# Performance work log

Measured on AMD Instinct MI355X. Metric: run time of the kernel, lower is better.

The kernel has to match this reference:

```python
import jax, jax.numpy as jnp
import numpy as np


def _u(k, shape, s):
    return jax.random.uniform(k, shape, jnp.float32, -s, s)


def setup_inputs() -> dict:
    B, T, F, H = 256, 256, 128, 256
    key = jax.random.key(0)
    ks = jax.random.split(key, 40)
    sH = 1.0 / np.sqrt(H).astype(np.float32)
    sF = 1.0 / np.sqrt(F).astype(np.float32)
    s2F = 1.0 / np.sqrt(2 * F).astype(np.float32)
    s3F = 1.0 / np.sqrt(3 * F).astype(np.float32)
    d = {
        'x': jax.random.normal(ks[0], (B, T, F), jnp.float32),
        'masking': (jax.random.uniform(ks[1], (B, T, F)) < 0.8).astype(jnp.float32),
        'time_lag': jax.random.uniform(ks[2], (B, T, F), jnp.float32),
        # forward LSTMCell (torch layout: W_ih [4H,2F], W_hh [4H,H], gates i,f,g,o)
        'fw_Wih': _u(ks[3], (4 * H, 2 * F), sH), 'fw_Whh': _u(ks[4], (4 * H, H), sH),
        'fw_bih': _u(ks[5], (4 * H,), sH), 'fw_bhh': _u(ks[6], (4 * H,), sH),
        'bw_Wih': _u(ks[7], (4 * H, 2 * F), sH), 'bw_Whh': _u(ks[8], (4 * H, H), sH),
        'bw_bih': _u(ks[9], (4 * H,), sH), 'bw_bhh': _u(ks[10], (4 * H,), sH),
        'fwlin_W': _u(ks[11], (F, H), sH), 'fwlin_b': _u(ks[12], (F,), sH),
        'bwlin_W': _u(ks[13], (F, H), sH), 'bwlin_b': _u(ks[14], (F,), sH),
        'fwz_W': _u(ks[15], (F, F), sF), 'fwz_b': _u(ks[16], (F,), sF),
        'bwz_W': _u(ks[17], (F, F), sF), 'bwz_b': _u(ks[18], (F,), sF),
        # beta linear 2F -> 3F
        'fwbeta_W': _u(ks[19], (3 * F, 2 * F), s2F), 'fwbeta_b': _u(ks[20], (3 * F,), s2F),
        'bwbeta_W': _u(ks[21], (3 * F, 2 * F), s2F), 'bwbeta_b': _u(ks[22], (3 * F,), s2F),
        # time-lag decay F -> H (both directions)
        'lag_W': _u(ks[23], (H, F), sF), 'lag_b': _u(ks[24], (H,), sF),
        'lagb_W': _u(ks[25], (H, F), sF), 'lagb_b': _u(ks[26], (H,), sF),
        # r_beta H -> F (both directions)
        'rbeta_W': _u(ks[27], (F, H), sH), 'rbeta_b': _u(ks[28], (F,), sH),
        'rbetab_W': _u(ks[29], (F, H), sH), 'rbetab_b': _u(ks[30], (F,), sH),
        # shared linear_layer_test 3F -> F
        'test_W': _u(ks[31], (F, 3 * F), s3F), 'test_b': _u(ks[32], (F,), s3F),
    }
    return d


def _lstm_cell(inp, h, c, Wih, Whh, bih, bhh):
    g = inp @ Wih.T + bih + h @ Whh.T + bhh
    i, f, gg, o = jnp.split(g, 4, axis=-1)
    c2 = jax.nn.sigmoid(f) * c + jax.nn.sigmoid(i) * jnp.tanh(gg)
    h2 = jax.nn.sigmoid(o) * jnp.tanh(c2)
    return h2, c2


def _run_dir(x, m, rr, rb, lin_W, lin_b, z_W, z_b, beta_W, beta_b, test_W, test_b, Wih, Whh, bih, bhh):
    # x, m: [T,B,F]; rr: [T,B,H]; rb: [T,B,F]
    F = x.shape[-1]
    offdiag = 1.0 - jnp.eye(F, dtype=x.dtype)

    def step(carry, inp):
        h, c = carry
        xj, mj, rj, rbj = inp
        out = h @ lin_W.T + lin_b                                 # [B,F]
        x_c = mj * xj + (1.0 - mj) * out
        z = x_c @ (z_W * offdiag).T + z_b
        beta = jax.nn.sigmoid(jnp.concatenate([mj, rbj], -1) @ beta_W.T + beta_b)
        beta = beta @ test_W.T + test_b                           # [B,F]
        c_val = beta * z + (1.0 - beta) * out
        c_c = mj * xj + (1.0 - mj) * c_val
        h2, c2 = _lstm_cell(jnp.concatenate([c_c, mj], -1), h * rj, c, Wih, Whh, bih, bhh)
        return (h2, c2), (out, z, c_val)

    bs, H = x.shape[1], Whh.shape[-1]
    h0 = jnp.zeros((bs, H), x.dtype)
    _, (outs, zs, cs) = jax.lax.scan(step, (h0, h0), (x, m, rr, rb))
    return outs, zs, cs


def reference(x, masking, time_lag, fw_Wih, fw_Whh, fw_bih, fw_bhh, bw_Wih, bw_Whh, bw_bih, bw_bhh, fwlin_W, fwlin_b, bwlin_W, bwlin_b, fwz_W, fwz_b, bwz_W, bwz_b, fwbeta_W, fwbeta_b, bwbeta_W, bwbeta_b, lag_W, lag_b, lagb_W, lagb_b, rbeta_W, rbeta_b, rbetab_W, rbetab_b, test_W, test_b):
    xt = jnp.transpose(x, (1, 0, 2))         # [T,B,F]
    mt = jnp.transpose(masking, (1, 0, 2))
    lt = jnp.transpose(time_lag, (1, 0, 2))
    # forward direction decay
    rr_f = jnp.exp(-jax.nn.relu(lt @ lag_W.T + lag_b))            # [T,B,H]
    rb_f = rr_f @ rbeta_W.T + rbeta_b                             # [T,B,F]
    of, zf, cf = _run_dir(xt, mt, rr_f, rb_f, fwlin_W, fwlin_b, fwz_W, fwz_b,
                          fwbeta_W, fwbeta_b, test_W, test_b, fw_Wih, fw_Whh, fw_bih, fw_bhh)
    # backward direction: iterate time reversed, then un-reverse outputs
    rr_b = jnp.exp(-jax.nn.relu(lt @ lagb_W.T + lagb_b))
    rb_b = rr_b @ rbetab_W.T + rbetab_b
    rev = lambda a: a[::-1]
    ob, zb, cb = _run_dir(rev(xt), rev(mt), rev(rr_b), rev(rb_b), bwlin_W, bwlin_b,
                          bwz_W, bwz_b, bwbeta_W, bwbeta_b, test_W, test_b,
                          bw_Wih, bw_Whh, bw_bih, bw_bhh)
    ob, zb, cb = rev(ob), rev(zb), rev(cb)
    perm = lambda a: jnp.transpose(a, (1, 0, 2))                  # back to [B,T,F]
    return (perm(of), perm(zf), perm(cf), perm(ob), perm(zb), perm(cb))
```

## Files before the change

### kernel.cpp

```cpp
#include <hip/hip_runtime.h>
#include <stdint.h>

#define TT 256
#define FF 128
#define HH 256
#define BB 256
#define BTc (BB * TT)
#define BTFc ((size_t)BB * TT * FF)

typedef __attribute__((ext_vector_type(8))) short short8;
typedef __attribute__((ext_vector_type(4))) float floatx4;
typedef __attribute__((ext_vector_type(4))) int intx4;

__device__ __forceinline__ floatx4 mfma16(short8 a, short8 b, floatx4 c) {
    return __builtin_amdgcn_mfma_f32_16x16x32_bf16(a, b, c, 0, 0, 0);
}
__device__ __forceinline__ intx4 mfmai8(long a, long b, intx4 c) {
    return __builtin_amdgcn_mfma_i32_16x16x32_i8(a, b, c, 0, 0, 0);
}

__device__ __forceinline__ float bf2f(short s) {
    return __uint_as_float(((unsigned)(unsigned short)s) << 16);
}
__device__ __forceinline__ short f2bf(float f) {
    unsigned u = __float_as_uint(f);
    u += 0x7FFFu + ((u >> 16) & 1u);
    return (short)(u >> 16);
}
__device__ __forceinline__ short8 ld_cvt8(const float* __restrict__ p) {
    short8 r;
#pragma unroll
    for (int j = 0; j < 8; ++j) r[j] = f2bf(p[j]);
    return r;
}
__device__ __forceinline__ float sigf(float x) { return 1.f / (1.f + __expf(-x)); }
__device__ __forceinline__ float tanhf_(float x) { return 1.f - 2.f / (1.f + __expf(2.f * x)); }

#define BARSYNC() do { asm volatile("s_waitcnt lgkmcnt(0)" ::: "memory"); \
                       __builtin_amdgcn_s_barrier(); } while (0)

struct PrepArgs {
    const float *s0, *s1, *s2, *s3, *s4, *s5, *s6;
    short *d0, *d1, *d2, *d3, *d4, *d5, *d6;
};
struct ScaleDesc { const float* src; int stride; int coloff; int K; int nrows; int sbase; };
struct ScaleArgs { ScaleDesc d[6]; float* s; };
struct PackBDesc { const float* src; short* dst; int stride; int coloff; int kts; int diag; int groups; };
struct AArgs { PrepArgs p; ScaleArgs s; PackBDesc b[6]; };

__global__ __launch_bounds__(256) void k_a(AArgs A) {
    if (blockIdx.x < 1472) {
        int i = blockIdx.x * 256 + threadIdx.x;
        const PrepArgs& P = A.p;
        if (i < 32768) { P.d0[i] = f2bf(P.s0[i]); return; }  i -= 32768;
        if (i < 32768) { P.d1[i] = f2bf(P.s1[i]); return; }  i -= 32768;
        if (i < 32768) { P.d2[i] = f2bf(P.s2[i]); return; }  i -= 32768;
        if (i < 32768) { P.d3[i] = f2bf(P.s3[i]); return; }  i -= 32768;
        if (i < 98304) { P.d4[i] = f2bf(P.s4[i]); return; }  i -= 98304;
        if (i < 98304) { P.d5[i] = f2bf(P.s5[i]); return; }  i -= 98304;
        if (i < 49152) { P.d6[i] = f2bf(P.s6[i]); return; }
        return;
    }
    if (blockIdx.x < 2560) {
        int gw = ((blockIdx.x - 1472) * 256 + threadIdx.x) >> 6;
        int lane = threadIdx.x & 63;
#pragma unroll 1
        for (int i = 0; i < 6; ++i) {
            if (gw < A.s.d[i].nrows) {
                const float* p = A.s.d[i].src + (size_t)gw * A.s.d[i].stride + A.s.d[i].coloff;
                float amax = 0.f;
                for (int j = lane; j < A.s.d[i].K; j += 64) amax = fmaxf(amax, fabsf(p[j]));
#pragma unroll
                for (int off = 32; off; off >>= 1) amax = fmaxf(amax, __shfl_xor(amax, off, 64));
                if (lane == 0) A.s.s[A.s.d[i].sbase + gw] = fmaxf(amax, 1e-20f);
                return;
            }
            gw -= A.s.d[i].nrows;
        }
        return;
    }
    int g = (blockIdx.x - 2560) * 256 + threadIdx.x;
#pragma unroll 1
    for (int i = 0; i < 6; ++i) {
        const PackBDesc& D = A.b[i];
        if (g < D.groups) {
            int frag = g >> 6, lane = g & 63;
            int nt = frag >> 2, kt = frag & 3;
            int ln = lane & 15, q4 = lane >> 4;
            int row = nt * 16 + ln;
            const float* p = D.src + (size_t)row * D.stride + D.coloff + kt * 32 + q4 * 8;
            short* dp = D.dst + (size_t)g * 8;
#pragma unroll
            for (int j = 0; j < 8; ++j) {
                int col = kt * 32 + q4 * 8 + j;
                float v = p[j];
                if (D.diag && col == row) v = 0.f;
                dp[j] = f2bf(v);
            }
            return;
        }
        g -= D.groups;
    }
}

struct PackQDesc { const float* src; char* dst; int stride; int coloff; int kts; int sbase; int groups; };
struct BArgs {
    const float* lt;
    const short* lagW0; const float* lagb0; const short* rbW0; const float* rbb0;
    short* rr0; short* rb0;
    const short* lagW1; const float* lagb1; const short* rbW1; const float* rbb1;
    short* rr1; short* rb1;
    const float* m;
    const short* wmB0; const short* wmB1;
    short* gb0; short* gb1;
    PackQDesc q[4]; const float* s;
};

__global__ __launch_bounds__(256) void k_b(BArgs A) {
    __shared__ short rrS[128][264];
    const int tid = threadIdx.x, lane = tid & 63, w = tid >> 6;
    const int ln = lane & 15, q4 = lane >> 4;

    if (blockIdx.x < 1024) {
        int b = blockIdx.x;
        const int dir = b >> 9; b &= 511;
        const int tc  = b & 7;
        const int q4d = (b >> 3) & 3;
        const int bg  = b >> 5;
        const short* lagW = dir ? A.lagW1 : A.lagW0;
        const float* lagb = dir ? A.lagb1 : A.lagb0;
        const short* rbW  = dir ? A.rbW1  : A.rbW0;
        const float* rbb  = dir ? A.rbb1  : A.rbb0;
        short* rr = dir ? A.rr1 : A.rr0;
        short* rb = dir ? A.rb1 : A.rb0;

#pragma unroll
        for (int mt = 0; mt < 2; ++mt) {
            const int rbase = w * 32 + mt * 16;
            floatx4 acc[16];
#pragma unroll
            for (int nt = 0; nt < 16; ++nt) { floatx4 z = {0.f, 0.f, 0.f, 0.f}; acc[nt] = z; }
            const int r = rbase + ln;
            const size_t aoff = ((size_t)(bg * 16 + q4d * 4 + (r >> 5)) * TT + tc * 32 + (r & 31)) * FF;
#pragma unroll
            for (int kt = 0; kt < 4; ++kt) {
                short8 a = ld_cvt8(A.lt + aoff + kt * 32 + q4 * 8);
#pragma unroll
                for (int nt = 0; nt < 16; ++nt) {
                    short8 bfr = *(const short8*)(lagW + (nt * 16 + ln) * 128 + kt * 32 + q4 * 8);
                    acc[nt] = mfma16(a, bfr, acc[nt]);
                }
            }
#pragma unroll
            for (int nt = 0; nt < 16; ++nt) {
                int n = nt * 16 + ln;
                float bias = lagb[n];
#pragma unroll
                for (int r2 = 0; r2 < 4; ++r2) {
                    int row = rbase + q4 * 4 + r2;
                    rrS[row][n] = f2bf(__expf(-fmaxf(acc[nt][r2] + bias, 0.f)));
                }
            }
        }
        __syncthreads();
        for (int c = tid; c < 32 * 256; c += 256) {
            int tl = c >> 8, n = c & 255;
            unsigned long long pk =
                ((unsigned long long)(unsigned short)rrS[tl][n]) |
                ((unsigned long long)(unsigned short)rrS[32 + tl][n] << 16) |
                ((unsigned long long)(unsigned short)rrS[64 + tl][n] << 32) |
                ((unsigned long long)(unsigned short)rrS[96 + tl][n] << 48);
            size_t doff = ((((size_t)(bg * TT + tc * 32 + tl) * 16 + (n >> 4)) * 64)
                           + q4d * 16 + (n & 15)) * 4;
            *(unsigned long long*)(rr + doff) = pk;
        }
#pragma unroll
        for (int mt = 0; mt < 2; ++mt) {
            const int rbase = w * 32 + mt * 16;
            floatx4 acc[8];
#pragma unroll
            for (int nt = 0; nt < 8; ++nt) { floatx4 z = {0.f, 0.f, 0.f, 0.f}; acc[nt] = z; }
#pragma unroll
            for (int kt = 0; kt < 8; ++kt) {
                short8 a = *(const short8*)&rrS[rbase + ln][kt * 32 + q4 * 8];
#pragma unroll
                for (int nt = 0; nt < 8; ++nt) {
                    short8 bfr = *(const short8*)(rbW + (nt * 16 + ln) * 256 + kt * 32 + q4 * 8);
                    acc[nt] = mfma16(a, bfr, acc[nt]);
                }
            }
#pragma unroll
            for (int nt = 0; nt < 8; ++nt) {
                int n = nt * 16 + ln;
                float bias = rbb[n];
#pragma unroll
                for (int r2 = 0; r2 < 4; ++r2) {
                    int row = rbase + q4 * 4 + r2;
                    size_t roff = ((size_t)(bg * 16 + q4d * 4 + (row >> 5)) * TT
                                   + tc * 32 + (row & 31)) * 128;
                    rb[roff + n] = f2bf(acc[nt][r2] + bias);
                }
            }
        }
        return;
    }

    if (blockIdx.x < 3072) {
        int task = (blockIdx.x - 1024) * 4 + w;
        const int dir = task >> 12; task &= 4095;
        const int bg = task >> 8, t = task & 255;
        const short* wB = dir ? A.wmB1 : A.wmB0;
        short* gb = dir ? A.gb1 : A.gb0;

        short8 a[4];
#pragma unroll
        for (int kt = 0; kt < 4; ++kt)
            a[kt] = ld_cvt8(A.m + ((size_t)(bg * 16 + ln) * TT + t) * FF + kt * 32 + q4 * 8);

        short* dst = gb + (size_t)task * 16384 + lane * 4;
#pragma unroll 2
        for (int nt = 0; nt < 64; ++nt) {
            floatx4 acc = {0.f, 0.f, 0.f, 0.f};
#pragma unroll
            for (int kt = 0; kt < 4; ++kt) {
                short8 bfr = *(const short8*)(wB + (nt * 4 + kt) * 512 + lane * 8);
                acc = mfma16(a[kt], bfr, acc);
            }
            unsigned long long pk =
                ((unsigned long long)(unsigned short)f2bf(acc[0])) |
                ((unsigned long long)(unsigned short)f2bf(acc[1]) << 16) |
                ((unsigned long long)(unsigned short)f2bf(acc[2]) << 32) |
                ((unsigned long long)(unsigned short)f2bf(acc[3]) << 48);
            *(unsigned long long*)(dst + nt * 256) = pk;
        }
        return;
    }

    int g = (blockIdx.x - 3072) * 256 + tid;
#pragma unroll 1
    for (int i = 0; i < 4; ++i) {
        const PackQDesc& D = A.q[i];
        if (g < D.groups) {
            int frag = g >> 6, plane = g & 63;
            int nt = frag / D.kts, kt = frag - nt * D.kts;
            int pln = plane & 15, pq4 = plane >> 4;
            int row = nt * 16 + pln;
            const float* p = D.src + (size_t)row * D.stride + D.coloff + kt * 32 + pq4 * 8;
            float inv = 127.f / A.s[D.sbase + row];
            char* dp = D.dst + (size_t)g * 8;
#pragma unroll
            for (int j = 0; j < 8; ++j) {
                int q = __float2int_rn(p[j] * inv);
                q = q > 127 ? 127 : (q < -127 ? -127 : q);
                dp[j] = (char)q;
            }
            return;
        }
        g -= D.groups;
    }
}

__global__ __launch_bounds__(256) void k_beta2(
    const float* __restrict__ m,
    const short* __restrict__ rb0, const short* __restrict__ rb1,
    const short* __restrict__ bW0, const short* __restrict__ bW1,
    const float* __restrict__ bb0, const float* __restrict__ bb1,
    const short* __restrict__ tW, const float* __restrict__ tb,
    short* __restrict__ bout0, short* __restrict__ bout1) {
    __shared__ short uS[64][392];
    const int tid = threadIdx.x, lane = tid & 63, w = tid >> 6;
    const int ln = lane & 15, q4 = lane >> 4;
    const int dir = blockIdx.x >> 10;
    const size_t r0 = (size_t)(blockIdx.x & 1023) * 64;
    const short* rb = dir ? rb1 : rb0;
    const short* bW = dir ? bW1 : bW0;
    const float* bb = dir ? bb1 : bb0;
    short* bout = dir ? bout1 : bout0;
    const int rbase = w * 16;

    {
        floatx4 acc[24];
#pragma unroll
        for (int nt = 0; nt < 24; ++nt) { floatx4 z = {0.f, 0.f, 0.f, 0.f}; acc[nt] = z; }
#pragma unroll
        for (int kt = 0; kt < 8; ++kt) {
            short8 a;
            if (kt < 4) a = ld_cvt8(m + (r0 + rbase + ln) * 128 + kt * 32 + q4 * 8);
            else        a = *(const short8*)(rb + (r0 + rbase + ln) * 128 + (kt - 4) * 32 + q4 * 8);
#pragma unroll
            for (int nt = 0; nt < 24; ++nt) {
                short8 b = *(const short8*)(bW + (nt * 16 + ln) * 256 + kt * 32 + q4 * 8);
                acc[nt] = mfma16(a, b, acc[nt]);
            }
        }
#pragma unroll
        for (int nt = 0; nt < 24; ++nt) {
            int n = nt * 16 + ln;
            float bias = bb[n];
#pragma unroll
            for (int r = 0; r < 4; ++r)
                uS[rbase + q4 * 4 + r][n] = f2bf(sigf(acc[nt][r] + bias));
        }
    }
    __syncthreads();
    {
        floatx4 acc[8];
#pragma unroll
        for (int nt = 0; nt < 8; ++nt) { floatx4 z = {0.f, 0.f, 0.f, 0.f}; acc[nt] = z; }
#pragma unroll
        for (int kt = 0; kt < 12; ++kt) {
            short8 a = *(const short8*)&uS[rbase + ln][kt * 32 + q4 * 8];
#pragma unroll
            for (int nt = 0; nt < 8; ++nt) {
                short8 b = *(const short8*)(tW + (nt * 16 + ln) * 384 + kt * 32 + q4 * 8);
                acc[nt] = mfma16(a, b, acc[nt]);
            }
        }
#pragma unroll
        for (int nt = 0; nt < 8; ++nt) {
            int n = nt * 16 + ln;
            float bias = tb[n];
#pragma unroll
            for (int r = 0; r < 4; ++r)
                bout[(r0 + rbase + q4 * 4 + r) * 128 + n] = f2bf(acc[nt][r] + bias);
        }
    }
}

struct ScanArgs {
    const float* x; const float* m;
    const short* rr0; const short* rr1;
    const short* beta0; const short* beta1;
    const short* gb0; const short* gb1;
    const char* whh0; const char* whh1;
    const char* lin0; const char* lin1;
    const short* wihc0; const short* wihc1;
    const short* zw0; const short* zw1;
    const float* s_all;
    const float* bih0; const float* bhh0; const float* bih1; const float* bhh1;
    const float* linb0; const float* linb1; const float* zb0; const float* zb1;
    float* out;
};

__global__ __launch_bounds__(1024, 4) void k_scan(ScanArgs A) {
    const int tid = threadIdx.x;
    const int lane = tid & 63;
    const int w = tid >> 6;
    const int ln = lane & 15;
    const int q4 = lane >> 4;
    const int dir = blockIdx.x >> 4;
    const int bgi = blockIdx.x & 15;
    const int bg0 = bgi * 16;

    const short* rrF   = dir ? A.rr1   : A.rr0;
    const short* beta  = dir ? A.beta1 : A.beta0;
    const short* gbF   = dir ? A.gb1   : A.gb0;
    const char*  whhQ  = dir ? A.whh1  : A.whh0;
    const char*  linQ  = dir ? A.lin1  : A.lin0;
    const short* wihcB = dir ? A.wihc1 : A.wihc0;
    const short* zwB   = dir ? A.zw1   : A.zw0;
    const float* bih   = dir ? A.bih1  : A.bih0;
    const float* bhh   = dir ? A.bhh1  : A.bhh0;
    const float* linb  = dir ? A.linb1 : A.linb0;
    const float* zb    = dir ? A.zb1   : A.zb0;
    const int so_whh  = dir ? 1024 : 0;
    const int so_lin  = 4096 + (dir ? 128 : 0);

    __shared__ char  hS8[16][264];
    __shared__ char  hrS8[16][264];
    __shared__ char  msS8[16][136];
    __shared__ short xS[16][136];
    __shared__ short bS[16][136];
    __shared__ short outS[16][136];
    __shared__ short ccS[16][136];
    __shared__ short zwS[16384];
    __shared__ char  linS8[32768];

    long WhhP[4][8];
#pragma unroll
    for (int q = 0; q < 4; ++q)
#pragma unroll
        for (int kt = 0; kt < 8; ++kt)
            WhhP[q][kt] = *(const long*)(whhQ + (((w + 16 * q) * 8 + kt) * 512 + lane * 8));

    float fhh[4], gb[4];
#pragma unroll
    for (int q = 0; q < 4; ++q) {
        int n = (w + 16 * q) * 16 + ln;
        fhh[q] = A.s_all[so_whh + n] * (1.f / 16129.f);
        gb[q]  = bih[n] + bhh[n];
    }
    float flin = 0.f, lb;
    if (w < 8) { int n = w * 16 + ln; flin = A.s_all[so_lin + n] * (1.f / 16129.f); lb = linb[n]; }
    else       { lb = zb[(w - 8) * 16 + ln]; }

    for (int i = tid; i < 16384; i += 1024) zwS[i] = zwB[i];
    for (int i = tid; i < 4096; i += 1024) ((long*)linS8)[i] = ((const long*)linQ)[i];
    for (int i = tid; i < 16 * 264; i += 1024) { hS8[i / 264][i % 264] = 0; hrS8[i / 264][i % 264] = 0; }

    auto GATES = [&](floatx4 (&g)[4], const long (&gq)[4]) {
#pragma unroll
        for (int pass = 0; pass < 2; ++pass) {
            const int q0 = pass * 2, q1 = pass * 2 + 1;
            intx4 gi0 = {0, 0, 0, 0}, gi1 = {0, 0, 0, 0};
#pragma unroll
            for (int kt = 0; kt < 8; ++kt) {
                long hrf = *(const long*)&hrS8[ln][kt * 32 + q4 * 8];
                gi0 = mfmai8(hrf, WhhP[q0][kt], gi0);
                gi1 = mfmai8(hrf, WhhP[q1][kt], gi1);
            }
#pragma unroll
            for (int r = 0; r < 4; ++r) {
                g[q0][r] = (float)gi0[r] * fhh[q0]
                         + bf2f((short)(((unsigned long long)gq[q0]) >> (16 * r))) + gb[q0];
                g[q1][r] = (float)gi1[r] * fhh[q1]
                         + bf2f((short)(((unsigned long long)gq[q1]) >> (16 * r))) + gb[q1];
            }
        }
    };

    const int tfirst = dir ? (TT - 1) : 0;
    {
        float2 xf = *(const float2*)(A.x + ((size_t)(bg0 + w) * TT + tfirst) * FF + lane * 2);
        float2 mf2 = *(const float2*)(A.m + ((size_t)(bg0 + w) * TT + tfirst) * FF + lane * 2);
        int    bf = *(const int*)(beta + ((size_t)(bg0 + w) * TT + tfirst) * FF + lane * 2);
        xS[w][lane * 2 + 0] = f2bf(xf.x);
        xS[w][lane * 2 + 1] = f2bf(xf.y);
        *(int*)&bS[w][lane * 2] = bf;
        msS8[w][lane * 2 + 0] = (char)(mf2.x != 0.f);
        msS8[w][lane * 2 + 1] = (char)(mf2.y != 0.f);
    }
    long gq[4];
#pragma unroll
    for (int q = 0; q < 4; ++q)
        gq[q] = *(const long*)(gbF + (((size_t)(bgi * TT + tfirst) * 64) + (w + 16 * q)) * 256
                                     + lane * 4);
    floatx4 cfr = {0.f, 0.f, 0.f, 0.f};
    __syncthreads();

    for (int tt = 0; tt < TT; ++tt) {
        const int t = dir ? (TT - 1 - tt) : tt;
        const int tn = dir ? (t > 0 ? t - 1 : 0) : (t < TT - 1 ? t + 1 : t);
        const size_t rowoffn = ((size_t)(bg0 + w) * TT + tn) * FF;

        float2 x_nxt = *(const float2*)(A.x + rowoffn + lane * 2);
        float2 m_nxt = *(const float2*)(A.m + rowoffn + lane * 2);
        int    b_nxt = *(const int*)(beta + rowoffn + lane * 2);
        unsigned long long rrv = *(const unsigned long long*)
            (rrF + ((((size_t)(bgi * TT + tn) * 16 + w) * 64) + lane) * 4);

        floatx4 g[4];
        if (w >= 8) {
            GATES(g, gq);
        } else {
            intx4 oi = {0, 0, 0, 0};
#pragma unroll
            for (int kt = 0; kt < 8; ++kt) {
                long lf = *(const long*)&linS8[(w * 8 + kt) * 512 + lane * 8];
                long hf = *(const long*)&hS8[ln][kt * 32 + q4 * 8];
                oi = mfmai8(hf, lf, oi);
            }
#pragma unroll
            for (int r = 0; r < 4; ++r)
                outS[q4 * 4 + r][w * 16 + ln] = f2bf((float)oi[r] * flin + lb);
        }
        BARSYNC();

        if (w >= 8) {
            floatx4 zv = {lb, lb, lb, lb};
#pragma unroll
            for (int kt = 0; kt < 4; ++kt) {
                const int c8 = kt * 32 + q4 * 8;
                short8 xv = *(const short8*)&xS[ln][c8];
                short8 ov = *(const short8*)&outS[ln][c8];
                unsigned long long mv = *(const unsigned long long*)&msS8[ln][c8];
                short8 xc;
#pragma unroll
                for (int j = 0; j < 8; ++j)
                    xc[j] = ((mv >> (8 * j)) & 0xffULL) ? xv[j] : ov[j];
                short8 zf = *(const short8*)&zwS[((w - 8) * 4 + kt) * 512 + lane * 8];
                zv = mfma16(xc, zf, zv);
            }
#pragma unroll
            for (int r = 0; r < 4; ++r) {
                const int row = q4 * 4 + r, col = (w - 8) * 16 + ln;
                short z16 = f2bf(zv[r]);
                float z0 = bf2f(z16);
                float o  = bf2f(outS[row][col]);
                float b  = bf2f(bS[row][col]);
                float cv = b * z0 + (1.f - b) * o;
                ccS[row][col] = msS8[row][col] ? xS[row][col] : f2bf(cv);
                size_t ob = (size_t)dir * 3 * BTFc + ((size_t)(bg0 + row) * TT + t) * FF + col;
                A.out[ob + BTFc]     = z0;
                A.out[ob + 2 * BTFc] = cv;
            }
        } else {
            {
                const int orow = 2 * w + (lane >> 5);
                const int ocol = (lane & 31) * 4;
                long ov4 = *(const long*)&outS[orow][ocol];
                float4 vo;
                vo.x = bf2f((short)(ov4));
                vo.y = bf2f((short)(ov4 >> 16));
                vo.z = bf2f((short)(ov4 >> 32));
                vo.w = bf2f((short)(ov4 >> 48));
                size_t ob = (size_t)dir * 3 * BTFc + ((size_t)(bg0 + orow) * TT + t) * FF + ocol;
                *(float4*)(A.out + ob) = vo;
            }
            GATES(g, gq);
        }
        BARSYNC();

#pragma unroll
        for (int q = 0; q < 4; ++q)
            gq[q] = *(const long*)(gbF + (((size_t)(bgi * TT + tn) * 64) + (w + 16 * q)) * 256
                                         + lane * 4);
#pragma unroll
        for (int kt = 0; kt < 4; ++kt) {
            short8 ccf = *(const short8*)&ccS[ln][kt * 32 + q4 * 8];
#pragma unroll
            for (int q = 0; q < 4; ++q) {
                short8 wc = *(const short8*)(wihcB + ((w + 16 * q) * 4 + kt) * 512 + lane * 8);
                g[q] = mfma16(ccf, wc, g[q]);
            }
        }
#pragma unroll
        for (int r = 0; r < 4; ++r) {
            float gi_ = g[0][r], gf_ = g[1][r], gg_ = g[2][r], go_ = g[3][r];
            float c2 = sigf(gf_) * cfr[r] + sigf(gi_) * tanhf_(gg_);
            float h2 = sigf(go_) * tanhf_(c2);
            cfr[r] = c2;
            float rv = bf2f((short)(rrv >> (16 * r)));
            hS8[q4 * 4 + r][w * 16 + ln]  = (char)__float2int_rn(h2 * 127.f);
            hrS8[q4 * 4 + r][w * 16 + ln] = (char)__float2int_rn(h2 * rv * 127.f);
        }
        xS[w][lane * 2 + 0] = f2bf(x_nxt.x);
        xS[w][lane * 2 + 1] = f2bf(x_nxt.y);
        *(int*)&bS[w][lane * 2] = b_nxt;
        msS8[w][lane * 2 + 0] = (char)(m_nxt.x != 0.f);
        msS8[w][lane * 2 + 1] = (char)(m_nxt.y != 0.f);
        BARSYNC();
    }
}

extern "C" void kernel_launch(void* const* d_in, const int* in_sizes, int n_in,
                              void* d_out, int out_size, void* d_ws, size_t ws_size,
                              hipStream_t stream) {
    (void)in_sizes; (void)n_in; (void)out_size; (void)ws_size;
    const float* x        = (const float*)d_in[0];
    const float* m        = (const float*)d_in[1];
    const float* lt       = (const float*)d_in[2];
    const float* fw_Wih   = (const float*)d_in[3];
    const float* fw_Whh   = (const float*)d_in[4];
    const float* fw_bih   = (const float*)d_in[5];
    const float* fw_bhh   = (const float*)d_in[6];
    const float* bw_Wih   = (const float*)d_in[7];
    const float* bw_Whh   = (const float*)d_in[8];
    const float* bw_bih   = (const float*)d_in[9];
    const float* bw_bhh   = (const float*)d_in[10];
    const float* fwlin_W  = (const float*)d_in[11];
    const float* fwlin_b  = (const float*)d_in[12];
    const float* bwlin_W  = (const float*)d_in[13];
    const float* bwlin_b  = (const float*)d_in[14];
    const float* fwz_W    = (const float*)d_in[15];
    const float* fwz_b    = (const float*)d_in[16];
    const float* bwz_W    = (const float*)d_in[17];
    const float* bwz_b    = (const float*)d_in[18];
    const float* fwbeta_W = (const float*)d_in[19];
    const float* fwbeta_b = (const float*)d_in[20];
    const float* bwbeta_W = (const float*)d_in[21];
    const float* bwbeta_b = (const float*)d_in[22];
    const float* lag_W    = (const float*)d_in[23];
    const float* lag_b    = (const float*)d_in[24];
    const float* lagb_W   = (const float*)d_in[25];
    const float* lagb_b   = (const float*)d_in[26];
    const float* rbeta_W  = (const float*)d_in[27];
    const float* rbeta_b  = (const float*)d_in[28];
    const float* rbetab_W = (const float*)d_in[29];
    const float* rbetab_b = (const float*)d_in[30];
    const float* test_W   = (const float*)d_in[31];
    const float* test_b   = (const float*)d_in[32];

    char* ws = (char*)d_ws;
    size_t o = 0;
    auto alloc = [&](size_t bytes) { char* p = ws + o; o += (bytes + 255) & ~(size_t)255; return p; };
    short* lagW0b  = (short*)alloc(65536);
    short* lagW1b  = (short*)alloc(65536);
    short* rbW0b   = (short*)alloc(65536);
    short* rbW1b   = (short*)alloc(65536);
    short* betaW0b = (short*)alloc(196608);
    short* betaW1b = (short*)alloc(196608);
    short* testWb  = (short*)alloc(98304);
    float* s_all   = (float*)alloc(4352 * 4);
    char*  whhQ0   = (char*)alloc(262144);
    char*  whhQ1   = (char*)alloc(262144);
    char*  linQ0   = (char*)alloc(32768);
    char*  linQ1   = (char*)alloc(32768);
    short* wihcB0  = (short*)alloc(262144);
    short* wihcB1  = (short*)alloc(262144);
    short* wihmB0  = (short*)alloc(262144);
    short* wihmB1  = (short*)alloc(262144);
    short* zwB0    = (short*)alloc(32768);
    short* zwB1    = (short*)alloc(32768);
    o = (o + ((size_t)1 << 20) - 1) & ~(((size_t)1 << 20) - 1);
    short* rr0 = (short*)(ws + o); o += (size_t)BTc * 256 * 2;
    short* rr1 = (short*)(ws + o); o += (size_t)BTc * 256 * 2;
    short* rb0 = (short*)(ws + o); o += (size_t)BTc * 128 * 2;
    short* rb1 = (short*)(ws + o); o += (size_t)BTc * 128 * 2;
    short* bt0 = (short*)(ws + o); o += (size_t)BTc * 128 * 2;
    short* bt1 = (short*)(ws + o); o += (size_t)BTc * 128 * 2;
    short* gb0 = (short*)(ws + o); o += (size_t)BTc * 1024 * 2;
    short* gb1 = (short*)(ws + o); o += (size_t)BTc * 1024 * 2;

    AArgs aa;
    aa.p.s0 = lag_W;    aa.p.d0 = lagW0b;
    aa.p.s1 = lagb_W;   aa.p.d1 = lagW1b;
    aa.p.s2 = rbeta_W;  aa.p.d2 = rbW0b;
    aa.p.s3 = rbetab_W; aa.p.d3 = rbW1b;
    aa.p.s4 = fwbeta_W; aa.p.d4 = betaW0b;
    aa.p.s5 = bwbeta_W; aa.p.d5 = betaW1b;
    aa.p.s6 = test_W;   aa.p.d6 = testWb;
    aa.s.d[0] = { fw_Whh,  256, 0,   256, 1024, 0 };
    aa.s.d[1] = { bw_Whh,  256, 0,   256, 1024, 1024 };
    aa.s.d[2] = { fw_Wih,  256, 128, 128, 1024, 2048 };
    aa.s.d[3] = { bw_Wih,  256, 128, 128, 1024, 3072 };
    aa.s.d[4] = { fwlin_W, 256, 0,   256, 128,  4096 };
    aa.s.d[5] = { bwlin_W, 256, 0,   256, 128,  4224 };
    aa.s.s = s_all;
    aa.b[0] = { fw_Wih, wihcB0, 256, 0,   4, 0, 16384 };
    aa.b[1] = { bw_Wih, wihcB1, 256, 0,   4, 0, 16384 };
    aa.b[2] = { fwz_W,  zwB0,   128, 0,   4, 1, 2048 };
    aa.b[3] = { bwz_W,  zwB1,   128, 0,   4, 1, 2048 };
    aa.b[4] = { fw_Wih, wihmB0, 256, 128, 4, 0, 16384 };
    aa.b[5] = { bw_Wih, wihmB1, 256, 128, 4, 0, 16384 };
    k_a<<<2832, 256, 0, stream>>>(aa);

    BArgs bb;
    bb.lt = lt;
    bb.lagW0 = lagW0b; bb.lagb0 = lag_b;  bb.rbW0 = rbW0b; bb.rbb0 = rbeta_b;
    bb.rr0 = rr0; bb.rb0 = rb0;
    bb.lagW1 = lagW1b; bb.lagb1 = lagb_b; bb.rbW1 = rbW1b; bb.rbb1 = rbetab_b;
    bb.rr1 = rr1; bb.rb1 = rb1;
    bb.m = m; bb.wmB0 = wihmB0; bb.wmB1 = wihmB1; bb.gb0 = gb0; bb.gb1 = gb1;
    bb.q[0] = { fw_Whh,  whhQ0,  256, 0,   8, 0,    32768 };
    bb.q[1] = { bw_Whh,  whhQ1,  256, 0,   8, 1024, 32768 };
    bb.q[2] = { fwlin_W, linQ0,  256, 0,   8, 4096, 4096 };
    bb.q[3] = { bwlin_W, linQ1,  256, 0,   8, 4224, 4096 };
    bb.s = s_all;
    k_b<<<3360, 256, 0, stream>>>(bb);

    k_beta2<<<2048, 256, 0, stream>>>(m, rb0, rb1, betaW0b, betaW1b,
                                      fwbeta_b, bwbeta_b, testWb, test_b, bt0, bt1);

    ScanArgs sa;
    sa.x = x; sa.m = m;
    sa.rr0 = rr0; sa.rr1 = rr1; sa.beta0 = bt0; sa.beta1 = bt1;
    sa.gb0 = gb0; sa.gb1 = gb1;
    sa.whh0 = whhQ0; sa.whh1 = whhQ1;
    sa.lin0 = linQ0; sa.lin1 = linQ1;
    sa.wihc0 = wihcB0; sa.wihc1 = wihcB1;
    sa.zw0 = zwB0; sa.zw1 = zwB1;
    sa.s_all = s_all;
    sa.bih0 = fw_bih; sa.bhh0 = fw_bhh; sa.bih1 = bw_bih; sa.bhh1 = bw_bhh;
    sa.linb0 = fwlin_b; sa.linb1 = bwlin_b; sa.zb0 = fwz_b; sa.zb1 = bwz_b;
    sa.out = (float*)d_out;
    k_scan<<<32, 1024, 0, stream>>>(sa);
}
```

Measured before the change: 4.919 ms.

## Halve beta kernel tile per block, strength-reduce scan pointers, split int8 accumulators

The beta precompute kernel now processes 32 rows per block, with each warp owning half of the output columns, and launches twice as many blocks. This cuts accumulator registers per thread to raise occupancy. The recurrent scan loop replaces per-step 64-bit index arithmetic with incrementing pointers for prefetches and output stores. It also splits the output-projection int8 MFMA chain into two independent accumulators to shorten the dependency chain. In exchange, the beta kernel now loads each weight B-fragment from twice as many blocks.

```diff
diff --git a/kernel.cpp b/kernel.cpp
--- a/kernel.cpp
+++ b/kernel.cpp
@@ -267,62 +267,65 @@
     const float* __restrict__ bb0, const float* __restrict__ bb1,
     const short* __restrict__ tW, const float* __restrict__ tb,
     short* __restrict__ bout0, short* __restrict__ bout1) {
-    __shared__ short uS[64][392];
+    __shared__ short uS[32][392];
     const int tid = threadIdx.x, lane = tid & 63, w = tid >> 6;
     const int ln = lane & 15, q4 = lane >> 4;
-    const int dir = blockIdx.x >> 10;
-    const size_t r0 = (size_t)(blockIdx.x & 1023) * 64;
+    const int dir = blockIdx.x >> 11;
+    const size_t r0 = (size_t)(blockIdx.x & 2047) * 32;
     const short* rb = dir ? rb1 : rb0;
     const short* bW = dir ? bW1 : bW0;
     const float* bb = dir ? bb1 : bb0;
     short* bout = dir ? bout1 : bout0;
-    const int rbase = w * 16;
+    const int rt = w >> 1;
+    const int nh = w & 1;
 
     {
-        floatx4 acc[24];
-#pragma unroll
-        for (int nt = 0; nt < 24; ++nt) { floatx4 z = {0.f, 0.f, 0.f, 0.f}; acc[nt] = z; }
+        floatx4 acc[12];
+#pragma unroll
+        for (int j = 0; j < 12; ++j) { floatx4 z = {0.f, 0.f, 0.f, 0.f}; acc[j] = z; }
 #pragma unroll
         for (int kt = 0; kt < 8; ++kt) {
             short8 a;
-            if (kt < 4) a = ld_cvt8(m + (r0 + rbase + ln) * 128 + kt * 32 + q4 * 8);
-            else        a = *(const short8*)(rb + (r0 + rbase + ln) * 128 + (kt - 4) * 32 + q4 * 8);
-#pragma unroll
-            for (int nt = 0; nt < 24; ++nt) {
+            if (kt < 4) a = ld_cvt8(m + (r0 + rt * 16 + ln) * 128 + kt * 32 + q4 * 8);
+            else        a = *(const short8*)(rb + (r0 + rt * 16 + ln) * 128 + (kt - 4) * 32 + q4 * 8);
+#pragma unroll
+            for (int j = 0; j < 12; ++j) {
+                int nt = nh * 12 + j;
                 short8 b = *(const short8*)(bW + (nt * 16 + ln) * 256 + kt * 32 + q4 * 8);
-                acc[nt] = mfma16(a, b, acc[nt]);
-            }
-        }
-#pragma unroll
-        for (int nt = 0; nt < 24; ++nt) {
-            int n = nt * 16 + ln;
+                acc[j] = mfma16(a, b, acc[j]);
+            }
+        }
+#pragma unroll
+        for (int j = 0; j < 12; ++j) {
+            int n = (nh * 12 + j) * 16 + ln;
             float bias = bb[n];
 #pragma unroll
             for (int r = 0; r < 4; ++r)
-                uS[rbase + q4 * 4 + r][n] = f2bf(sigf(acc[nt][r] + bias));
+                uS[rt * 16 + q4 * 4 + r][n] = f2bf(sigf(acc[j][r] + bias));
         }
     }
     __syncthreads();
     {
-        floatx4 acc[8];
-#pragma unroll
-        for (int nt = 0; nt < 8; ++nt) { floatx4 z = {0.f, 0.f, 0.f, 0.f}; acc[nt] = z; }
+        floatx4 acc[4];
+#pragma unroll
+        for (int j = 0; j < 4; ++j) { floatx4 z = {0.f, 0.f, 0.f, 0.f}; acc[j] = z; }
 #pragma unroll
         for (int kt = 0; kt < 12; ++kt) {
-            short8 a = *(const short8*)&uS[rbase + ln][kt * 32 + q4 * 8];
-#pragma unroll
-            for (int nt = 0; nt < 8; ++nt) {
+            short8 a = *(const short8*)&uS[rt * 16 + ln][kt * 32 + q4 * 8];
+#pragma unroll
+            for (int j = 0; j < 4; ++j) {
+                int nt = nh * 4 + j;
                 short8 b = *(const short8*)(tW + (nt * 16 + ln) * 384 + kt * 32 + q4 * 8);
-                acc[nt] = mfma16(a, b, acc[nt]);
-            }
-        }
-#pragma unroll
-        for (int nt = 0; nt < 8; ++nt) {
-            int n = nt * 16 + ln;
+                acc[j] = mfma16(a, b, acc[j]);
+            }
+        }
+#pragma unroll
+        for (int j = 0; j < 4; ++j) {
+            int n = (nh * 4 + j) * 16 + ln;
             float bias = tb[n];
 #pragma unroll
             for (int r = 0; r < 4; ++r)
-                bout[(r0 + rbase + q4 * 4 + r) * 128 + n] = f2bf(acc[nt][r] + bias);
+                bout[(r0 + rt * 16 + q4 * 4 + r) * 128 + n] = f2bf(acc[j][r] + bias);
         }
     }
 }
@@ -420,6 +423,7 @@
     };
 
     const int tfirst = dir ? (TT - 1) : 0;
+    const int tsec   = dir ? (TT - 2) : 1;
     {
         float2 xf = *(const float2*)(A.x + ((size_t)(bg0 + w) * TT + tfirst) * FF + lane * 2);
         float2 mf2 = *(const float2*)(A.m + ((size_t)(bg0 + w) * TT + tfirst) * FF + lane * 2);
@@ -435,34 +439,47 @@
     for (int q = 0; q < 4; ++q)
         gq[q] = *(const long*)(gbF + (((size_t)(bgi * TT + tfirst) * 64) + (w + 16 * q)) * 256
                                      + lane * 4);
+
+    const int sgn = dir ? -1 : 1;
+    const float* pXn = A.x  + ((size_t)(bg0 + w) * TT + tsec) * FF + lane * 2;
+    const float* pMn = A.m  + ((size_t)(bg0 + w) * TT + tsec) * FF + lane * 2;
+    const short* pBn = beta + ((size_t)(bg0 + w) * TT + tsec) * FF + lane * 2;
+    const short* pRRn = rrF + ((((size_t)(bgi * TT + tsec) * 16 + w) * 64) + lane) * 4;
+    const short* pGQn = gbF + ((size_t)(bgi * TT + tsec) * 64 + w) * 256 + lane * 4;
+    float* pO   = A.out + (size_t)dir * 3 * BTFc
+                + ((size_t)(bg0 + 2 * w + (lane >> 5)) * TT + tfirst) * FF + (lane & 31) * 4;
+    float* pZCV = A.out + (size_t)dir * 3 * BTFc
+                + ((size_t)(bg0 + q4 * 4) * TT + tfirst) * FF + (w - 8) * 16 + ln;
+    const int dF  = sgn * FF;
+    const int dRR = sgn * 4096;
+    const int dGQ = sgn * 16384;
+
     floatx4 cfr = {0.f, 0.f, 0.f, 0.f};
     __syncthreads();
 
     for (int tt = 0; tt < TT; ++tt) {
-        const int t = dir ? (TT - 1 - tt) : tt;
-        const int tn = dir ? (t > 0 ? t - 1 : 0) : (t < TT - 1 ? t + 1 : t);
-        const size_t rowoffn = ((size_t)(bg0 + w) * TT + tn) * FF;
-
-        float2 x_nxt = *(const float2*)(A.x + rowoffn + lane * 2);
-        float2 m_nxt = *(const float2*)(A.m + rowoffn + lane * 2);
-        int    b_nxt = *(const int*)(beta + rowoffn + lane * 2);
-        unsigned long long rrv = *(const unsigned long long*)
-            (rrF + ((((size_t)(bgi * TT + tn) * 16 + w) * 64) + lane) * 4);
+        float2 x_nxt = *(const float2*)pXn;
+        float2 m_nxt = *(const float2*)pMn;
+        int    b_nxt = *(const int*)pBn;
+        unsigned long long rrv = *(const unsigned long long*)pRRn;
 
         floatx4 g[4];
         if (w >= 8) {
             GATES(g, gq);
         } else {
-            intx4 oi = {0, 0, 0, 0};
-#pragma unroll
-            for (int kt = 0; kt < 8; ++kt) {
-                long lf = *(const long*)&linS8[(w * 8 + kt) * 512 + lane * 8];
-                long hf = *(const long*)&hS8[ln][kt * 32 + q4 * 8];
-                oi = mfmai8(hf, lf, oi);
+            intx4 oi0 = {0, 0, 0, 0}, oi1 = {0, 0, 0, 0};
+#pragma unroll
+            for (int kt = 0; kt < 4; ++kt) {
+                long lf0 = *(const long*)&linS8[(w * 8 + kt) * 512 + lane * 8];
+                long hf0 = *(const long*)&hS8[ln][kt * 32 + q4 * 8];
+                oi0 = mfmai8(hf0, lf0, oi0);
+                long lf1 = *(const long*)&linS8[(w * 8 + 4 + kt) * 512 + lane * 8];
+                long hf1 = *(const long*)&hS8[ln][(4 + kt) * 32 + q4 * 8];
+                oi1 = mfmai8(hf1, lf1, oi1);
             }
 #pragma unroll
             for (int r = 0; r < 4; ++r)
-                outS[q4 * 4 + r][w * 16 + ln] = f2bf((float)oi[r] * flin + lb);
+                outS[q4 * 4 + r][w * 16 + ln] = f2bf((float)(oi0[r] + oi1[r]) * flin + lb);
         }
         BARSYNC();
 
@@ -490,9 +507,9 @@
                 float b  = bf2f(bS[row][col]);
                 float cv = b * z0 + (1.f - b) * o;
                 ccS[row][col] = msS8[row][col] ? xS[row][col] : f2bf(cv);
-                size_t ob = (size_t)dir * 3 * BTFc + ((size_t)(bg0 + row) * TT + t) * FF + col;
-                A.out[ob + BTFc]     = z0;
-                A.out[ob + 2 * BTFc] = cv;
+                float* pr = pZCV + (size_t)r * (TT * FF);
+                pr[BTFc]     = z0;
+                pr[2 * BTFc] = cv;
             }
         } else {
             {
@@ -504,8 +521,7 @@
                 vo.y = bf2f((short)(ov4 >> 16));
                 vo.z = bf2f((short)(ov4 >> 32));
                 vo.w = bf2f((short)(ov4 >> 48));
-                size_t ob = (size_t)dir * 3 * BTFc + ((size_t)(bg0 + orow) * TT + t) * FF + ocol;
-                *(float4*)(A.out + ob) = vo;
+                *(float4*)pO = vo;
             }
             GATES(g, gq);
         }
@@ -513,8 +529,7 @@
 
 #pragma unroll
         for (int q = 0; q < 4; ++q)
-            gq[q] = *(const long*)(gbF + (((size_t)(bgi * TT + tn) * 64) + (w + 16 * q)) * 256
-                                         + lane * 4);
+            gq[q] = *(const long*)(pGQn + q * 4096);
 #pragma unroll
         for (int kt = 0; kt < 4; ++kt) {
             short8 ccf = *(const short8*)&ccS[ln][kt * 32 + q4 * 8];
@@ -539,6 +554,12 @@
         *(int*)&bS[w][lane * 2] = b_nxt;
         msS8[w][lane * 2 + 0] = (char)(m_nxt.x != 0.f);
         msS8[w][lane * 2 + 1] = (char)(m_nxt.y != 0.f);
+
+        pO += dF; pZCV += dF;
+        if (tt < TT - 2) {
+            pXn += dF; pMn += dF; pBn += dF;
+            pRRn += dRR; pGQn += dGQ;
+        }
         BARSYNC();
     }
 }
@@ -649,7 +670,7 @@
     bb.s = s_all;
     k_b<<<3360, 256, 0, stream>>>(bb);
 
-    k_beta2<<<2048, 256, 0, stream>>>(m, rb0, rb1, betaW0b, betaW1b,
+    k_beta2<<<4096, 256, 0, stream>>>(m, rb0, rb1, betaW0b, betaW1b,
                                       fwbeta_b, bwbeta_b, testWb, test_b, bt0, bt1);
 
     ScanArgs sa;
```

Measured after the change: 5.050 ms. 2.7% more time.
